# Performance work log

Hardware: AMD Instinct MI355X
Metric: run time of the kernel (lower is better)

## Reference

```python
import jax, jax.numpy as jnp
import numpy as np

E, H = 1024, 16
N, S, T = 2, 2048, 2048


def setup_inputs() -> dict:
    key = jax.random.key(0)
    ks = jax.random.split(key, 8)
    scale = 1.0 / np.sqrt(E)
    q = jax.random.normal(ks[0], (N, S, E), dtype=jnp.float32)
    k = jax.random.normal(ks[1], (N, T, E), dtype=jnp.float32)
    v = jax.random.normal(ks[2], (N, T, E), dtype=jnp.float32)
    pad_mask = jax.random.randint(ks[3], (N, 1, 1, T), 0, 2, dtype=jnp.int32)
    subsq_mask = jnp.tril(jnp.ones((S, T), dtype=jnp.int32))[None, None]
    Wq = jax.random.normal(ks[4], (E, E), dtype=jnp.float32) * scale
    Wk = jax.random.normal(ks[5], (E, E), dtype=jnp.float32) * scale
    Wv = jax.random.normal(ks[6], (E, E), dtype=jnp.float32) * scale
    bq = jnp.zeros((E,), dtype=jnp.float32)
    bk = jnp.zeros((E,), dtype=jnp.float32)
    bv = jnp.zeros((E,), dtype=jnp.float32)
    return {"query": q, "key": k, "value": v, "pad_mask": pad_mask,
            "subsq_mask": subsq_mask, "Wq": Wq, "bq": bq, "Wk": Wk,
            "bk": bk, "Wv": Wv, "bv": bv}


def reference(query, key, value, pad_mask, subsq_mask, Wq, bq, Wk, bk, Wv, bv):
    n, s, e = query.shape
    t = value.shape[1]
    d = e // H
    # Linear projections (torch Linear: x @ W^T + b), split into heads
    q = (query @ Wq.T + bq).reshape(n, s, H, d).transpose(0, 2, 1, 3)  # [N,H,S,D]
    k = (key @ Wk.T + bk).reshape(n, t, H, d).transpose(0, 2, 1, 3)    # [N,H,T,D]
    v = (value @ Wv.T + bv).reshape(n, t, H, d).transpose(0, 2, 1, 3)  # [N,H,T,D]
    att = jnp.einsum('bhsd,bhtd->bhst', q, k) / jnp.sqrt(jnp.float32(d))
    att = jnp.where(pad_mask == 0, jnp.float32(-1e9), att)
    att = jnp.where(subsq_mask == 0, jnp.float32(-1e9), att)
    prob = jax.nn.softmax(att, axis=-1)
    out = jnp.einsum('bhst,bhtd->bhsd', prob, v)  # [N,H,S,D]
    return out.transpose(0, 2, 1, 3).reshape(n, s, e)
```

## Files before the change

### kernel.cpp

```cpp
#include <hip/hip_runtime.h>

#define HEADS 16
#define DH    64
#define EMB   1024
#define NBAT  2
#define SEQ   2048
#define KDIM  1024
#define NROW  (NBAT * SEQ)

typedef __attribute__((ext_vector_type(8))) short short8;
typedef __attribute__((ext_vector_type(4))) short short4v;
typedef __attribute__((ext_vector_type(4))) float floatx4;
typedef unsigned short u16;
typedef unsigned int   u32;
typedef unsigned long long u64;

__device__ __forceinline__ u16 f2bf(float x) {
    u32 u = __builtin_bit_cast(u32, x);
    u += 0x7fffu + ((u >> 16) & 1u);
    return (u16)(u >> 16);
}
__device__ __forceinline__ float bf2f(u16 v) {
    return __builtin_bit_cast(float, ((u32)v) << 16);
}

__device__ __forceinline__ void gll16(const u16* g, u16* l) {
    __builtin_amdgcn_global_load_lds((const __attribute__((address_space(1))) u32*)g,
                                     (__attribute__((address_space(3))) u32*)l, 16, 0, 0);
}

__global__ __launch_bounds__(256) void cvt_kernel(
    const float* __restrict__ q, const float* __restrict__ k, const float* __restrict__ v,
    const float* __restrict__ wq, const float* __restrict__ wk, const float* __restrict__ wv,
    u16* __restrict__ xb, u16* __restrict__ wb)
{
    const int z = blockIdx.y;
    const float* src; u16* dst; int n;
    if (z < 3) { src = (z == 0) ? q : (z == 1) ? k : v;     dst = xb + (size_t)z * 4194304;       n = 4194304; }
    else       { src = (z == 3) ? wq : (z == 4) ? wk : wv;  dst = wb + (size_t)(z - 3) * 1048576; n = 1048576; }
    for (int i = (blockIdx.x * 256 + threadIdx.x) * 8; i < n; i += 512 * 256 * 8) {
        float4 a = *(const float4*)(src + i);
        float4 b = *(const float4*)(src + i + 4);
        short8 o;
        o[0] = (short)f2bf(a.x); o[1] = (short)f2bf(a.y); o[2] = (short)f2bf(a.z); o[3] = (short)f2bf(a.w);
        o[4] = (short)f2bf(b.x); o[5] = (short)f2bf(b.y); o[6] = (short)f2bf(b.z); o[7] = (short)f2bf(b.w);
        *(short8*)(dst + i) = o;
    }
}

__global__ __launch_bounds__(256) void proj_kernel(
    const u16* __restrict__ xb, const u16* __restrict__ wb,
    const float* __restrict__ bq, const float* __restrict__ bk, const float* __restrict__ bv,
    u16* __restrict__ qh, u16* __restrict__ kh, u16* __restrict__ vt)
{
    const int f = blockIdx.x;
    const int xcd = f & 7, jj = f >> 3;
    const int g  = xcd * 12 + (jj >> 3);
    const int nx = jj & 7;
    const int z  = g >> 5, y = g & 31;

    const u16* A  = xb + (size_t)z * 4194304;
    const u16* B  = wb + (size_t)z * 1048576;
    const float* Bp = (z == 0) ? bq : (z == 1) ? bk : bv;
    u16* dst        = (z == 0) ? qh : (z == 1) ? kh : vt;

    const int m0 = y * 128;
    const int n0 = nx * 128;
    const int tid  = threadIdx.x;
    const int wave = tid >> 6, lane = tid & 63;
    const int quad = lane >> 4, l15 = lane & 15;
    const int waveM = wave >> 1, waveN = wave & 1;

    __shared__ __align__(16) u16 smem[2 * 128 * 64];
    u16* As = smem;
    u16* Bs = smem + 128 * 64;

    floatx4 acc[4][4];
    for (int a = 0; a < 4; a++)
        for (int b = 0; b < 4; b++)
            acc[a][b] = floatx4{0.f, 0.f, 0.f, 0.f};

    const int lrow = lane >> 3, lcol = (lane & 7) * 8;

    for (int k0 = 0; k0 < KDIM; k0 += 64) {
        for (int j = 0; j < 4; j++) {
            int r8 = wave * 32 + j * 8;
            gll16(A + (size_t)(m0 + r8 + lrow) * KDIM + k0 + lcol, &As[r8 * 64]);
        }
        for (int j = 0; j < 4; j++) {
            int r8 = wave * 32 + j * 8;
            gll16(B + (size_t)(n0 + r8 + lrow) * KDIM + k0 + lcol, &Bs[r8 * 64]);
        }
        __syncthreads();

        for (int ks = 0; ks < 2; ks++) {
            short8 af[4], bfg[4];
            for (int mb = 0; mb < 4; mb++)
                af[mb]  = *(const short8*)&As[(waveM * 64 + mb * 16 + l15) * 64 + ks * 32 + quad * 8];
            for (int nb = 0; nb < 4; nb++)
                bfg[nb] = *(const short8*)&Bs[(waveN * 64 + nb * 16 + l15) * 64 + ks * 32 + quad * 8];
            for (int mb = 0; mb < 4; mb++)
                for (int nb = 0; nb < 4; nb++)
                    acc[mb][nb] = __builtin_amdgcn_mfma_f32_16x16x32_bf16(af[mb], bfg[nb], acc[mb][nb], 0, 0, 0);
        }
        __syncthreads();
    }

    if (z != 2) {
        const int row0 = m0 + waveM * 64;
        const int col0 = n0 + waveN * 64;
        const float scale = (z == 0) ? 0.125f : 1.0f;
        for (int nb = 0; nb < 4; nb++) {
            int col = col0 + nb * 16 + l15;
            float bias = Bp[col];
            int hh = col >> 6, dd = col & 63;
            for (int mb = 0; mb < 4; mb++) {
                for (int r = 0; r < 4; r++) {
                    int row = row0 + mb * 16 + quad * 4 + r;
                    int nn = row >> 11, ss = row & 2047;
                    dst[((size_t)(nn * HEADS + hh) * SEQ + ss) * DH + dd] =
                        f2bf((acc[mb][nb][r] + bias) * scale);
                }
            }
        }
    } else {
        const int nn  = m0 >> 11;
        const int ss0 = m0 & 2047;
        for (int p = 0; p < 2; p++) {
            if (waveN == p) {
                for (int nb = 0; nb < 4; nb++) {
                    int col_l = nb * 16 + l15;
                    float bias = Bp[n0 + p * 64 + col_l];
                    for (int mb = 0; mb < 4; mb++) {
                        short4v pk;
                        for (int r = 0; r < 4; r++)
                            pk[r] = (short)f2bf(acc[mb][nb][r] + bias);
                        *(short4v*)&smem[col_l * 136 + waveM * 64 + mb * 16 + quad * 4] = pk;
                    }
                }
            }
            __syncthreads();
            const int hh = (n0 >> 6) + p;
            u16* drow = dst + ((size_t)(nn * HEADS + hh) * DH) * SEQ + ss0;
            for (int c2 = tid; c2 < 1024; c2 += 256) {
                int dl = c2 >> 4, tc = (c2 & 15) * 8;
                short8 vv = *(const short8*)&smem[dl * 136 + tc];
                *(short8*)(drow + (size_t)dl * SEQ + tc) = vv;
            }
            __syncthreads();
        }
    }
}

__global__ __launch_bounds__(256) void vmean_kernel(const u16* __restrict__ vt,
                                                    float* __restrict__ vmean)
{
    const int row = blockIdx.x;
    const u16* p = vt + (size_t)row * SEQ;
    const int tid = threadIdx.x;
    float s = 0.f;
    for (int i = tid; i < SEQ; i += 256) s += bf2f(p[i]);
    __shared__ float red[256];
    red[tid] = s;
    __syncthreads();
    for (int st = 128; st > 0; st >>= 1) {
        if (tid < st) red[tid] += red[tid + st];
        __syncthreads();
    }
    if (tid == 0) vmean[row] = red[0] * (1.f / (float)SEQ);
}

__global__ __launch_bounds__(256) void attn_kernel(
    const u16* __restrict__ qh, const u16* __restrict__ kh, const u16* __restrict__ vt,
    const int* __restrict__ pad, const float* __restrict__ vmean,
    float* __restrict__ out)
{
    const int f = blockIdx.x;
    const int xcd = f & 7, jj = f >> 3;
    const int nh = xcd * 4 + (jj >> 4);
    const int pr = jj & 15;
    const int n = nh >> 4, h = nh & 15;
    const int tid  = threadIdx.x;
    const int wave = tid >> 6, lane = tid & 63;
    const int quad = lane >> 4, l15 = lane & 15;

    __shared__ __align__(16) u16 Ks[2][64 * 72];
    __shared__ __align__(16) u16 Vs[2][64 * 72];
    __shared__ __align__(16) u16 Ps[64 * 72];
    __shared__ u64 padb[32];

    {
        const int* pp = pad + n * SEQ;
        for (int i = 0; i < 8; i++) {
            int seg = wave * 8 + i;
            u64 m = __ballot(pp[seg * 64 + lane] != 0);
            if (lane == 0) padb[seg] = m;
        }
    }

    const u16* qbase = qh + (size_t)nh * SEQ * DH;
    const u16* kbase = kh + (size_t)nh * SEQ * DH;
    const u16* vbase = vt + (size_t)nh * DH * SEQ;

    short8 ones;
    for (int i = 0; i < 8; i++) ones[i] = (short)0x3F80;
    float vm[4];
    for (int nd = 0; nd < 4; nd++) vm[nd] = vmean[nh * DH + nd * 16 + l15];

    for (int half = 0; half < 2; half++) {
        const int sb = half ? (31 - pr) : pr;
        const int s0 = sb * 64;
        const int nt = sb + 1;
        const int srow = s0 + wave * 16 + l15;

        short8 qf[2];
        for (int ks = 0; ks < 2; ks++)
            qf[ks] = *(const short8*)(qbase + (size_t)srow * DH + ks * 32 + quad * 8);

        floatx4 oacc[4], lacc;
        for (int nd = 0; nd < 4; nd++) oacc[nd] = floatx4{0.f, 0.f, 0.f, 0.f};
        lacc = floatx4{0.f, 0.f, 0.f, 0.f};

        short8 rK[2], rV[2];
        for (int i = 0; i < 2; i++) {
            int idx = i * 256 + tid, row = idx >> 3, c = (idx & 7) * 8;
            rK[i] = *(const short8*)(kbase + (size_t)row * DH + c);
            rV[i] = *(const short8*)(vbase + (size_t)row * SEQ + c);
        }
        __syncthreads();

        for (int tb = 0; tb < nt; tb++) {
            const int cur = tb & 1;
            for (int i = 0; i < 2; i++) {
                int idx = i * 256 + tid, row = idx >> 3, c = (idx & 7) * 8;
                *(short8*)&Ks[cur][row * 72 + c] = rK[i];
                *(short8*)&Vs[cur][row * 72 + c] = rV[i];
            }
            if (tb + 1 < nt) {
                const int t0n = (tb + 1) * 64;
                for (int i = 0; i < 2; i++) {
                    int idx = i * 256 + tid, row = idx >> 3, c = (idx & 7) * 8;
                    rK[i] = *(const short8*)(kbase + (size_t)(t0n + row) * DH + c);
                    rV[i] = *(const short8*)(vbase + (size_t)row * SEQ + t0n + c);
                }
            }
            __syncthreads();

            const int t0 = tb * 64;
            const u64 w = padb[t0 >> 6];
            const bool diag = (tb == sb);

            floatx4 sc[4];
            for (int nb = 0; nb < 4; nb++) sc[nb] = floatx4{0.f, 0.f, 0.f, 0.f};
            for (int ks = 0; ks < 2; ks++)
                for (int nb = 0; nb < 4; nb++) {
                    short8 kf = *(const short8*)&Ks[cur][(nb * 16 + l15) * 72 + ks * 32 + quad * 8];
                    sc[nb] = __builtin_amdgcn_mfma_f32_16x16x32_bf16(kf, qf[ks], sc[nb], 0, 0, 0);
                }

            for (int nb = 0; nb < 4; nb++) {
                short4v pk;
                for (int r = 0; r < 4; r++) {
                    int sh = nb * 16 + quad * 4 + r;
                    bool ok = ((w >> sh) & 1ull) != 0;
                    if (diag) ok = ok && (t0 + sh <= srow);
                    float p = ok ? __expf(sc[nb][r]) : 0.f;
                    pk[r] = (short)f2bf(p);
                }
                *(short4v*)&Ps[(wave * 16 + l15) * 72 + nb * 16 + quad * 4] = pk;
            }
            asm volatile("s_waitcnt lgkmcnt(0)" ::: "memory");

            for (int ks = 0; ks < 2; ks++) {
                short8 pa = *(const short8*)&Ps[(wave * 16 + l15) * 72 + ks * 32 + quad * 8];
                for (int nd = 0; nd < 4; nd++) {
                    short8 vb = *(const short8*)&Vs[cur][(nd * 16 + l15) * 72 + ks * 32 + quad * 8];
                    oacc[nd] = __builtin_amdgcn_mfma_f32_16x16x32_bf16(pa, vb, oacc[nd], 0, 0, 0);
                }
                lacc = __builtin_amdgcn_mfma_f32_16x16x32_bf16(pa, ones, lacc, 0, 0, 0);
            }
        }

        for (int r = 0; r < 4; r++) {
            float l = lacc[r];
            int s = s0 + wave * 16 + quad * 4 + r;
            float* orow = out + (size_t)(n * SEQ + s) * EMB + h * DH;
            if (l > 0.f) {
                float inv = 1.f / l;
                for (int nd = 0; nd < 4; nd++) orow[nd * 16 + l15] = oacc[nd][r] * inv;
            } else {
                for (int nd = 0; nd < 4; nd++) orow[nd * 16 + l15] = vm[nd];
            }
        }
    }
}

extern "C" void kernel_launch(void* const* d_in, const int* in_sizes, int n_in,
                              void* d_out, int out_size, void* d_ws, size_t ws_size,
                              hipStream_t stream)
{
    const float* qin = (const float*)d_in[0];
    const float* kin = (const float*)d_in[1];
    const float* vin = (const float*)d_in[2];
    const int*   pad = (const int*)d_in[3];
    const float* Wq = (const float*)d_in[5];
    const float* bq = (const float*)d_in[6];
    const float* Wk = (const float*)d_in[7];
    const float* bk = (const float*)d_in[8];
    const float* Wv = (const float*)d_in[9];
    const float* bv = (const float*)d_in[10];
    float* out = (float*)d_out;

    const size_t per = (size_t)NBAT * HEADS * SEQ * DH;
    u16* qh = (u16*)d_ws;
    u16* kh = qh + per;
    u16* vt = kh + per;
    float* vmean = (float*)(vt + per);
    u16* xb = (u16*)(vmean + 2048);
    u16* wb = xb + 3 * per;

    cvt_kernel<<<dim3(512, 6), 256, 0, stream>>>(qin, kin, vin, Wq, Wk, Wv, xb, wb);
    proj_kernel<<<dim3(768), 256, 0, stream>>>(xb, wb, bq, bk, bv, qh, kh, vt);
    vmean_kernel<<<dim3(NBAT * HEADS * DH), 256, 0, stream>>>(vt, vmean);
    attn_kernel<<<dim3(512), 256, 0, stream>>>(qh, kh, vt, pad, vmean, out);
}
```

Before: 230.9 us.

## XOR-swizzle LDS tiles and use direct global-to-LDS loads in attention

Applies an XOR swizzle to the 16-byte column chunks of the GEMM and attention LDS tiles so that MFMA fragment reads avoid bank conflicts without padding. The attention kernel now loads K/V tiles with direct global-to-LDS loads into a double buffer, replacing the register staging path, and the sync point moves to the top of the loop. It also folds log2(e) into the Q scale so the softmax can use the hardware exp2 instruction. The risks are correctness of the swizzle index math and whether async load completion is properly waited on before the barrier.

```diff
diff --git a/kernel.cpp b/kernel.cpp
--- a/kernel.cpp
+++ b/kernel.cpp
@@ -70,6 +70,7 @@
     const int wave = tid >> 6, lane = tid & 63;
     const int quad = lane >> 4, l15 = lane & 15;
     const int waveM = wave >> 1, waveN = wave & 1;
+    const int sw = l15 & 7;
 
     __shared__ __align__(16) u16 smem[2 * 128 * 64];
     u16* As = smem;
@@ -80,25 +81,26 @@
         for (int b = 0; b < 4; b++)
             acc[a][b] = floatx4{0.f, 0.f, 0.f, 0.f};
 
-    const int lrow = lane >> 3, lcol = (lane & 7) * 8;
+    const int lrow = lane >> 3;
+    const int gcol = ((lane & 7) ^ lrow) * 8;
 
     for (int k0 = 0; k0 < KDIM; k0 += 64) {
         for (int j = 0; j < 4; j++) {
             int r8 = wave * 32 + j * 8;
-            gll16(A + (size_t)(m0 + r8 + lrow) * KDIM + k0 + lcol, &As[r8 * 64]);
+            gll16(A + (size_t)(m0 + r8 + lrow) * KDIM + k0 + gcol, &As[r8 * 64]);
         }
         for (int j = 0; j < 4; j++) {
             int r8 = wave * 32 + j * 8;
-            gll16(B + (size_t)(n0 + r8 + lrow) * KDIM + k0 + lcol, &Bs[r8 * 64]);
+            gll16(B + (size_t)(n0 + r8 + lrow) * KDIM + k0 + gcol, &Bs[r8 * 64]);
         }
         __syncthreads();
 
         for (int ks = 0; ks < 2; ks++) {
             short8 af[4], bfg[4];
             for (int mb = 0; mb < 4; mb++)
-                af[mb]  = *(const short8*)&As[(waveM * 64 + mb * 16 + l15) * 64 + ks * 32 + quad * 8];
+                af[mb]  = *(const short8*)&As[(waveM * 64 + mb * 16 + l15) * 64 + ((ks * 4 + quad) ^ sw) * 8];
             for (int nb = 0; nb < 4; nb++)
-                bfg[nb] = *(const short8*)&Bs[(waveN * 64 + nb * 16 + l15) * 64 + ks * 32 + quad * 8];
+                bfg[nb] = *(const short8*)&Bs[(waveN * 64 + nb * 16 + l15) * 64 + ((ks * 4 + quad) ^ sw) * 8];
             for (int mb = 0; mb < 4; mb++)
                 for (int nb = 0; nb < 4; nb++)
                     acc[mb][nb] = __builtin_amdgcn_mfma_f32_16x16x32_bf16(af[mb], bfg[nb], acc[mb][nb], 0, 0, 0);
@@ -109,7 +111,7 @@
     if (z != 2) {
         const int row0 = m0 + waveM * 64;
         const int col0 = n0 + waveN * 64;
-        const float scale = (z == 0) ? 0.125f : 1.0f;
+        const float scale = (z == 0) ? 0.125f * 1.44269504f : 1.0f;
         for (int nb = 0; nb < 4; nb++) {
             int col = col0 + nb * 16 + l15;
             float bias = Bp[col];
@@ -183,9 +185,10 @@
     const int tid  = threadIdx.x;
     const int wave = tid >> 6, lane = tid & 63;
     const int quad = lane >> 4, l15 = lane & 15;
-
-    __shared__ __align__(16) u16 Ks[2][64 * 72];
-    __shared__ __align__(16) u16 Vs[2][64 * 72];
+    const int sw = l15 & 7;
+
+    __shared__ __align__(16) u16 Ks[2][64 * 64];
+    __shared__ __align__(16) u16 Vs[2][64 * 64];
     __shared__ __align__(16) u16 Ps[64 * 72];
     __shared__ u64 padb[32];
 
@@ -207,6 +210,9 @@
     float vm[4];
     for (int nd = 0; nd < 4; nd++) vm[nd] = vmean[nh * DH + nd * 16 + l15];
 
+    const int lrow = lane >> 3;
+    const int gcol = ((lane & 7) ^ lrow) * 8;
+
     for (int half = 0; half < 2; half++) {
         const int sb = half ? (31 - pr) : pr;
         const int s0 = sb * 64;
@@ -221,30 +227,26 @@
         for (int nd = 0; nd < 4; nd++) oacc[nd] = floatx4{0.f, 0.f, 0.f, 0.f};
         lacc = floatx4{0.f, 0.f, 0.f, 0.f};
 
-        short8 rK[2], rV[2];
-        for (int i = 0; i < 2; i++) {
-            int idx = i * 256 + tid, row = idx >> 3, c = (idx & 7) * 8;
-            rK[i] = *(const short8*)(kbase + (size_t)row * DH + c);
-            rV[i] = *(const short8*)(vbase + (size_t)row * SEQ + c);
-        }
         __syncthreads();
+
+        for (int j = 0; j < 2; j++) {
+            int r8 = wave * 16 + j * 8;
+            gll16(kbase + (size_t)(r8 + lrow) * DH + gcol, &Ks[0][r8 * 64]);
+            gll16(vbase + (size_t)(r8 + lrow) * SEQ + gcol, &Vs[0][r8 * 64]);
+        }
 
         for (int tb = 0; tb < nt; tb++) {
             const int cur = tb & 1;
-            for (int i = 0; i < 2; i++) {
-                int idx = i * 256 + tid, row = idx >> 3, c = (idx & 7) * 8;
-                *(short8*)&Ks[cur][row * 72 + c] = rK[i];
-                *(short8*)&Vs[cur][row * 72 + c] = rV[i];
-            }
+            __syncthreads();
+
             if (tb + 1 < nt) {
                 const int t0n = (tb + 1) * 64;
-                for (int i = 0; i < 2; i++) {
-                    int idx = i * 256 + tid, row = idx >> 3, c = (idx & 7) * 8;
-                    rK[i] = *(const short8*)(kbase + (size_t)(t0n + row) * DH + c);
-                    rV[i] = *(const short8*)(vbase + (size_t)row * SEQ + t0n + c);
-                }
-            }
-            __syncthreads();
+                for (int j = 0; j < 2; j++) {
+                    int r8 = wave * 16 + j * 8;
+                    gll16(kbase + (size_t)(t0n + r8 + lrow) * DH + gcol, &Ks[1 - cur][r8 * 64]);
+                    gll16(vbase + (size_t)(r8 + lrow) * SEQ + t0n + gcol, &Vs[1 - cur][r8 * 64]);
+                }
+            }
 
             const int t0 = tb * 64;
             const u64 w = padb[t0 >> 6];
@@ -254,7 +256,7 @@
             for (int nb = 0; nb < 4; nb++) sc[nb] = floatx4{0.f, 0.f, 0.f, 0.f};
             for (int ks = 0; ks < 2; ks++)
                 for (int nb = 0; nb < 4; nb++) {
-                    short8 kf = *(const short8*)&Ks[cur][(nb * 16 + l15) * 72 + ks * 32 + quad * 8];
+                    short8 kf = *(const short8*)&Ks[cur][(nb * 16 + l15) * 64 + ((ks * 4 + quad) ^ sw) * 8];
                     sc[nb] = __builtin_amdgcn_mfma_f32_16x16x32_bf16(kf, qf[ks], sc[nb], 0, 0, 0);
                 }
 
@@ -264,7 +266,7 @@
                     int sh = nb * 16 + quad * 4 + r;
                     bool ok = ((w >> sh) & 1ull) != 0;
                     if (diag) ok = ok && (t0 + sh <= srow);
-                    float p = ok ? __expf(sc[nb][r]) : 0.f;
+                    float p = ok ? __builtin_amdgcn_exp2f(sc[nb][r]) : 0.f;
                     pk[r] = (short)f2bf(p);
                 }
                 *(short4v*)&Ps[(wave * 16 + l15) * 72 + nb * 16 + quad * 4] = pk;
@@ -274,7 +276,7 @@
             for (int ks = 0; ks < 2; ks++) {
                 short8 pa = *(const short8*)&Ps[(wave * 16 + l15) * 72 + ks * 32 + quad * 8];
                 for (int nd = 0; nd < 4; nd++) {
-                    short8 vb = *(const short8*)&Vs[cur][(nd * 16 + l15) * 72 + ks * 32 + quad * 8];
+                    short8 vb = *(const short8*)&Vs[cur][(nd * 16 + l15) * 64 + ((ks * 4 + quad) ^ sw) * 8];
                     oacc[nd] = __builtin_amdgcn_mfma_f32_16x16x32_bf16(pa, vb, oacc[nd], 0, 0, 0);
                 }
                 lacc = __builtin_amdgcn_mfma_f32_16x16x32_bf16(pa, ones, lacc, 0, 0, 0);
```

After: 216.4 us. 6.3% less time.
